# Performance work log

Measured on AMD Instinct MI355X. Metric: run time of the kernel, lower is better.

## Reference

```python
import jax, jax.numpy as jnp
import numpy as np

N_HEAD = 8
HEAD_DIM = 64  # d_model // n_head
NEG = -1000000000.0  # diagonal mask fill


def _rope(x):
    # x: [B, H, T, D], interleaved RoPE as in torch module
    T, D = x.shape[-2], x.shape[-1]
    theta = 1.0 / (10000.0 ** (jnp.arange(0, D, 2, dtype=jnp.float32) / D))  # [D/2]
    angle = jnp.arange(T, dtype=jnp.float32)[:, None] * theta[None, :]        # [T, D/2]
    cos, sin = jnp.cos(angle), jnp.sin(angle)
    x1, x2 = x[..., ::2], x[..., 1::2]
    # stack on last axis then flatten -> interleave
    out = jnp.stack([x1 * cos - x2 * sin, x1 * sin + x2 * cos], axis=-1)
    return out.reshape(x.shape)


def setup_inputs() -> dict:
    key = jax.random.key(0)
    k1, k2, k3 = jax.random.split(key, 3)
    B, T, C = 4, 2048, 512
    x = jax.random.normal(k1, (B, T, C), dtype=jnp.float32)
    w_qkv = jax.random.normal(k2, (C, 3 * C), dtype=jnp.float32) * 0.02
    w_proj = jax.random.normal(k3, (C, C), dtype=jnp.float32) * 0.02
    return {"x": x, "w_qkv": w_qkv, "w_proj": w_proj}


def reference(x, w_qkv, w_proj):
    B, T, C = x.shape
    H, D = N_HEAD, HEAD_DIM
    qkv = jnp.einsum('btc,cd->btd', x, w_qkv)
    q, k, v = jnp.split(qkv, 3, axis=-1)
    q = q.reshape(B, T, H, D).transpose(0, 2, 1, 3)
    k = k.reshape(B, T, H, D).transpose(0, 2, 1, 3)
    v = v.reshape(B, T, H, D).transpose(0, 2, 1, 3)
    q = _rope(q)
    k = _rope(k)
    scale = 1.0 / jnp.sqrt(jnp.float32(D))
    scores = jnp.einsum('bhqd,bhkd->bhqk', q, k) * scale
    mask = jnp.where(jnp.eye(T, dtype=bool), jnp.float32(NEG), jnp.float32(0.0))
    scores = scores + mask
    attn = jax.nn.softmax(scores, axis=-1)
    y = jnp.einsum('bhqk,bhkd->bhqd', attn, v)
    y = y.transpose(0, 2, 1, 3).reshape(B, T, C)
    return jnp.einsum('btc,cd->btd', y, w_proj)
```

## Files before the change

kernel.cpp:

```cpp
#include <hip/hip_runtime.h>

typedef unsigned short u16;
typedef __bf16 bf16x8 __attribute__((ext_vector_type(8)));
typedef float f32x4 __attribute__((ext_vector_type(4)));

#define B_ 4
#define T_ 2048
#define C_ 512
#define H_ 8
#define D_ 64

__device__ __forceinline__ u16 f2bf(float f) {
  unsigned u = __float_as_uint(f);
  unsigned r = (u + 0x7FFFu + ((u >> 16) & 1u)) >> 16;
  return (u16)r;
}
__device__ __forceinline__ float bf2f(unsigned h) {
  return __uint_as_float(h << 16);
}
__device__ __forceinline__ void gload16(const u16* g, u16* l) {
  __builtin_amdgcn_global_load_lds(
      (const __attribute__((address_space(1))) unsigned int*)g,
      (__attribute__((address_space(3))) unsigned int*)l, 16, 0, 0);
}

__global__ void cast4_kernel(const float* __restrict__ in, u16* __restrict__ out) {
  int i = blockIdx.x * blockDim.x + threadIdx.x;
  float4 v = ((const float4*)in)[i];
  unsigned lo = (unsigned)f2bf(v.x) | ((unsigned)f2bf(v.y) << 16);
  unsigned hi = (unsigned)f2bf(v.z) | ((unsigned)f2bf(v.w) << 16);
  ((uint2*)out)[i] = make_uint2(lo, hi);
}

__global__ void castT_kernel(const float* __restrict__ in, u16* __restrict__ outT,
                             int R, int Cc) {
  int i = blockIdx.x * blockDim.x + threadIdx.x;
  if (i >= R * Cc) return;
  int r = i / Cc, c = i - r * Cc;
  outT[c * R + r] = f2bf(in[i]);
}

__global__ void rope_table_kernel(float* __restrict__ cosT, float* __restrict__ sinT) {
  int i = blockIdx.x * blockDim.x + threadIdx.x;
  int t = i >> 5, p = i & 31;
  float theta = powf(10000.f, -(float)p / 32.f);
  float a = (float)t * theta;
  cosT[i] = cosf(a);
  sinT[i] = sinf(a);
}

__global__ void rope_kernel(u16* __restrict__ Qp, u16* __restrict__ Kp,
                            const float* __restrict__ cosT, const float* __restrict__ sinT) {
  int i = blockIdx.x * blockDim.x + threadIdx.x;
  int p = i & 31;
  int t = (i >> 5) & 2047;
  int bh = (i >> 16) & 31;
  u16* base = (i >> 21) ? Kp : Qp;
  unsigned off = ((unsigned)(bh * 2048 + t)) * 64u + (unsigned)(p * 2);
  unsigned v = *(const unsigned*)&base[off];
  int ti = (t << 5) + p;
  float c = cosT[ti], s = sinT[ti];
  float x1 = bf2f(v & 0xFFFFu), x2 = bf2f(v >> 16);
  float o1 = x1 * c - x2 * s;
  float o2 = x1 * s + x2 * c;
  *(unsigned*)&base[off] = (unsigned)f2bf(o1) | ((unsigned)f2bf(o2) << 16);
}

template <int EPI>
__global__ __launch_bounds__(256, 2)
void gemm_bt_kernel(const u16* __restrict__ A, const u16* __restrict__ BT,
                    int M, int N, int K, float* __restrict__ Cout,
                    u16* __restrict__ Qp, u16* __restrict__ Kp, u16* __restrict__ VTp) {
  __shared__ u16 As[128 * 64];
  __shared__ u16 Bs[128 * 64];
  const int tid = threadIdx.x;
  const int w = tid >> 6, l = tid & 63;
  const int m0 = blockIdx.x * 128, n0 = blockIdx.y * 128;
  const int wr = w >> 1, wc = w & 1;
  f32x4 acc[4][4] = {};

  const int srow = w * 32 + (l >> 3);
  const int scol = (l & 7) * 8;

  for (int k0 = 0; k0 < K; k0 += 64) {
#pragma unroll
    for (int c = 0; c < 4; ++c) {
      gload16(A + (m0 + srow + c * 8) * K + k0 + scol, &As[(w * 32 + c * 8) * 64]);
      gload16(BT + (n0 + srow + c * 8) * K + k0 + scol, &Bs[(w * 32 + c * 8) * 64]);
    }
    __syncthreads();
#pragma unroll
    for (int kk = 0; kk < 2; ++kk) {
      bf16x8 af[4], bfr[4];
#pragma unroll
      for (int i = 0; i < 4; ++i)
        af[i] = *(const bf16x8*)&As[(wr * 64 + i * 16 + (l & 15)) * 64 + kk * 32 + (l >> 4) * 8];
#pragma unroll
      for (int j = 0; j < 4; ++j)
        bfr[j] = *(const bf16x8*)&Bs[(wc * 64 + j * 16 + (l & 15)) * 64 + kk * 32 + (l >> 4) * 8];
#pragma unroll
      for (int i = 0; i < 4; ++i)
#pragma unroll
        for (int j = 0; j < 4; ++j)
          acc[i][j] = __builtin_amdgcn_mfma_f32_16x16x32_bf16(af[i], bfr[j], acc[i][j], 0, 0, 0);
    }
    __syncthreads();
  }

  const int mrow = wr * 64 + (l >> 4) * 4;
  const int ncol = wc * 64 + (l & 15);
  if (EPI == 1) {
#pragma unroll
    for (int i = 0; i < 4; ++i)
#pragma unroll
      for (int j = 0; j < 4; ++j)
#pragma unroll
        for (int r = 0; r < 4; ++r)
          Cout[(m0 + mrow + i * 16 + r) * N + (n0 + ncol + j * 16)] = acc[i][j][r];
  } else {
#pragma unroll
    for (int i = 0; i < 4; ++i) {
#pragma unroll
      for (int j = 0; j < 4; ++j) {
        int n = n0 + ncol + j * 16;
        int which = n >> 9;
        int hn = n & 511;
        int h = hn >> 6, d = hn & 63;
#pragma unroll
        for (int r = 0; r < 4; ++r) {
          int m = m0 + mrow + i * 16 + r;
          int b = m >> 11, t = m & 2047;
          int bh = b * 8 + h;
          u16 v = f2bf(acc[i][j][r]);
          if (which == 0)
            Qp[(bh * 2048 + t) * 64 + d] = v;
          else if (which == 1)
            Kp[(bh * 2048 + t) * 64 + d] = v;
          else
            VTp[(bh * 64 + d) * 2048 + t] = v;
        }
      }
    }
  }
}

__global__ __launch_bounds__(256, 2)
void attn_kernel(const u16* __restrict__ Qp, const u16* __restrict__ Kp,
                 const u16* __restrict__ VTp, u16* __restrict__ Yp) {
  __shared__ u16 Ks[64 * 64];
  __shared__ u16 Vs[64 * 64];
  __shared__ u16 Ps[4 * 16 * 64];
  const int tid = threadIdx.x;
  const int w = tid >> 6, l = tid & 63;
  const int qt = blockIdx.x, bh = blockIdx.y;
  const int b = bh >> 3, h = bh & 7;
  const int q0 = qt * 64;
  const u16* Qb = Qp + (bh * 2048 + q0) * 64;
  const u16* Kb = Kp + bh * 2048 * 64;
  const u16* Vb = VTp + bh * 64 * 2048;

  bf16x8 qf[2];
  {
    int row = w * 16 + (l & 15);
#pragma unroll
    for (int kk = 0; kk < 2; ++kk)
      qf[kk] = *(const bf16x8*)&Qb[row * 64 + kk * 32 + (l >> 4) * 8];
  }
  f32x4 o[4] = {};
  float dsum[4] = {0.f, 0.f, 0.f, 0.f};

  const int srow = w * 16 + (l >> 3);
  const int scol = ((l & 7) ^ (l >> 3)) * 8;
  const int rsw  = (l & 7) << 3;

  for (int kt = 0; kt < 32; ++kt) {
#pragma unroll
    for (int c = 0; c < 2; ++c) {
      gload16(Kb + (kt * 64 + srow + c * 8) * 64 + scol, &Ks[(w * 16 + c * 8) * 64]);
      gload16(Vb + (srow + c * 8) * 2048 + kt * 64 + scol, &Vs[(w * 16 + c * 8) * 64]);
    }
    __syncthreads();

#pragma unroll
    for (int nt = 0; nt < 4; ++nt) {
      f32x4 s = {0.f, 0.f, 0.f, 0.f};
#pragma unroll
      for (int kk = 0; kk < 2; ++kk) {
        bf16x8 kf = *(const bf16x8*)&Ks[(nt * 16 + (l & 15)) * 64 +
                                        ((kk * 32 + (l >> 4) * 8) ^ rsw)];
        s = __builtin_amdgcn_mfma_f32_16x16x32_bf16(qf[kk], kf, s, 0, 0, 0);
      }
      int key = kt * 64 + nt * 16 + (l & 15);
#pragma unroll
      for (int r = 0; r < 4; ++r) {
        int q = q0 + w * 16 + (l >> 4) * 4 + r;
        float p = (q == key) ? 0.f : __expf(s[r] * 0.125f);
        dsum[r] += p;
        int prow = w * 16 + (l >> 4) * 4 + r;
        Ps[prow * 64 + ((nt * 16 + (l & 15)) ^ ((prow & 7) << 3))] = f2bf(p);
      }
    }
    __syncthreads();

#pragma unroll
    for (int nt = 0; nt < 4; ++nt) {
#pragma unroll
      for (int kk = 0; kk < 2; ++kk) {
        bf16x8 pf = *(const bf16x8*)&Ps[(w * 16 + (l & 15)) * 64 +
                                        ((kk * 32 + (l >> 4) * 8) ^ rsw)];
        bf16x8 vf = *(const bf16x8*)&Vs[(nt * 16 + (l & 15)) * 64 +
                                        ((kk * 32 + (l >> 4) * 8) ^ rsw)];
        o[nt] = __builtin_amdgcn_mfma_f32_16x16x32_bf16(pf, vf, o[nt], 0, 0, 0);
      }
    }
    __syncthreads();
  }

#pragma unroll
  for (int m = 1; m < 16; m <<= 1)
#pragma unroll
    for (int r = 0; r < 4; ++r)
      dsum[r] += __shfl_xor(dsum[r], m, 64);

  float inv[4];
#pragma unroll
  for (int r = 0; r < 4; ++r) inv[r] = 1.f / dsum[r];

#pragma unroll
  for (int nt = 0; nt < 4; ++nt)
#pragma unroll
    for (int r = 0; r < 4; ++r) {
      int t = q0 + w * 16 + (l >> 4) * 4 + r;
      int cc = h * 64 + nt * 16 + (l & 15);
      Yp[(b * 2048 + t) * 512 + cc] = f2bf(o[nt][r] * inv[r]);
    }
}

extern "C" void kernel_launch(void* const* d_in, const int* in_sizes, int n_in,
                              void* d_out, int out_size, void* d_ws, size_t ws_size,
                              hipStream_t stream) {
  const float* x = (const float*)d_in[0];
  const float* wqkv = (const float*)d_in[1];
  const float* wproj = (const float*)d_in[2];
  float* out = (float*)d_out;
  char* ws = (char*)d_ws;

  u16* xb     = (u16*)(ws);
  u16* Yp     = (u16*)(ws);
  u16* wqkvT  = (u16*)(ws + 8388608);
  u16* wprojT = (u16*)(ws + 9961472);
  u16* Qp     = (u16*)(ws + 10485760);
  u16* Kp     = (u16*)(ws + 18874368);
  u16* VTp    = (u16*)(ws + 27262976);
  float* cosT = (float*)(ws + 35651584);
  float* sinT = (float*)(ws + 35913728);

  cast4_kernel<<<4096, 256, 0, stream>>>(x, xb);
  castT_kernel<<<3072, 256, 0, stream>>>(wqkv, wqkvT, 512, 1536);
  castT_kernel<<<1024, 256, 0, stream>>>(wproj, wprojT, 512, 512);
  rope_table_kernel<<<256, 256, 0, stream>>>(cosT, sinT);

  gemm_bt_kernel<0><<<dim3(64, 12), 256, 0, stream>>>(xb, wqkvT, 8192, 1536, 512,
                                                      nullptr, Qp, Kp, VTp);
  rope_kernel<<<16384, 256, 0, stream>>>(Qp, Kp, cosT, sinT);
  attn_kernel<<<dim3(32, 32), 256, 0, stream>>>(Qp, Kp, VTp, Yp);
  gemm_bt_kernel<1><<<dim3(64, 4), 256, 0, stream>>>(Yp, wprojT, 8192, 512, 512,
                                                     out, nullptr, nullptr, nullptr);
}
```

Measured before the change: 199.3 us.

## Double-buffer K/V tiles in attention and drop the mid-loop barrier

The attention loop now prefetches the next K/V tile into a second LDS buffer while the current tile is being computed, instead of loading and waiting at the top of each iteration. The barrier between writing P and reading it back is removed, since each wave only reads its own P rows. The diagonal-mask test now runs only on the diagonal tile. The weight-transpose cast kernel is also changed to write its output coalesced. The cost is double the LDS for K/V, which could reduce occupancy, and the design depends on the end-of-iteration barrier waiting for the async LDS loads.

```diff
diff --git a/kernel.cpp b/kernel.cpp
--- a/kernel.cpp
+++ b/kernel.cpp
@@ -36,8 +36,8 @@
                              int R, int Cc) {
   int i = blockIdx.x * blockDim.x + threadIdx.x;
   if (i >= R * Cc) return;
-  int r = i / Cc, c = i - r * Cc;
-  outT[c * R + r] = f2bf(in[i]);
+  int c = i / R, r = i - c * R;
+  outT[i] = f2bf(in[r * Cc + c]);
 }
 
 __global__ void rope_table_kernel(float* __restrict__ cosT, float* __restrict__ sinT) {
@@ -147,8 +147,8 @@
 __global__ __launch_bounds__(256, 2)
 void attn_kernel(const u16* __restrict__ Qp, const u16* __restrict__ Kp,
                  const u16* __restrict__ VTp, u16* __restrict__ Yp) {
-  __shared__ u16 Ks[64 * 64];
-  __shared__ u16 Vs[64 * 64];
+  __shared__ u16 Ks[2][64 * 64];
+  __shared__ u16 Vs[2][64 * 64];
   __shared__ u16 Ps[4 * 16 * 64];
   const int tid = threadIdx.x;
   const int w = tid >> 6, l = tid & 63;
@@ -173,34 +173,44 @@
   const int scol = ((l & 7) ^ (l >> 3)) * 8;
   const int rsw  = (l & 7) << 3;
 
+#define STAGE(kt, bb)                                                            \
+  do {                                                                           \
+    _Pragma("unroll")                                                            \
+    for (int c = 0; c < 2; ++c) {                                                \
+      gload16(Kb + ((kt) * 64 + srow + c * 8) * 64 + scol,                       \
+              &Ks[bb][(w * 16 + c * 8) * 64]);                                   \
+      gload16(Vb + (srow + c * 8) * 2048 + (kt) * 64 + scol,                     \
+              &Vs[bb][(w * 16 + c * 8) * 64]);                                   \
+    }                                                                            \
+  } while (0)
+
+  STAGE(0, 0);
+  __syncthreads();
+
+  int cur = 0;
   for (int kt = 0; kt < 32; ++kt) {
-#pragma unroll
-    for (int c = 0; c < 2; ++c) {
-      gload16(Kb + (kt * 64 + srow + c * 8) * 64 + scol, &Ks[(w * 16 + c * 8) * 64]);
-      gload16(Vb + (srow + c * 8) * 2048 + kt * 64 + scol, &Vs[(w * 16 + c * 8) * 64]);
-    }
-    __syncthreads();
+    if (kt < 31) STAGE(kt + 1, cur ^ 1);
+    const bool diagtile = (kt == qt);
 
 #pragma unroll
     for (int nt = 0; nt < 4; ++nt) {
       f32x4 s = {0.f, 0.f, 0.f, 0.f};
 #pragma unroll
       for (int kk = 0; kk < 2; ++kk) {
-        bf16x8 kf = *(const bf16x8*)&Ks[(nt * 16 + (l & 15)) * 64 +
-                                        ((kk * 32 + (l >> 4) * 8) ^ rsw)];
+        bf16x8 kf = *(const bf16x8*)&Ks[cur][(nt * 16 + (l & 15)) * 64 +
+                                           ((kk * 32 + (l >> 4) * 8) ^ rsw)];
         s = __builtin_amdgcn_mfma_f32_16x16x32_bf16(qf[kk], kf, s, 0, 0, 0);
       }
-      int key = kt * 64 + nt * 16 + (l & 15);
+      int keyi = nt * 16 + (l & 15);
 #pragma unroll
       for (int r = 0; r < 4; ++r) {
-        int q = q0 + w * 16 + (l >> 4) * 4 + r;
-        float p = (q == key) ? 0.f : __expf(s[r] * 0.125f);
-        dsum[r] += p;
-        int prow = w * 16 + (l >> 4) * 4 + r;
-        Ps[prow * 64 + ((nt * 16 + (l & 15)) ^ ((prow & 7) << 3))] = f2bf(p);
-      }
-    }
-    __syncthreads();
+        int qrow = w * 16 + (l >> 4) * 4 + r;
+        float e = __expf(s[r] * 0.125f);
+        if (diagtile && (qrow == keyi)) e = 0.f;
+        dsum[r] += e;
+        Ps[qrow * 64 + (keyi ^ ((qrow & 7) << 3))] = f2bf(e);
+      }
+    }
 
 #pragma unroll
     for (int nt = 0; nt < 4; ++nt) {
@@ -208,13 +218,15 @@
       for (int kk = 0; kk < 2; ++kk) {
         bf16x8 pf = *(const bf16x8*)&Ps[(w * 16 + (l & 15)) * 64 +
                                         ((kk * 32 + (l >> 4) * 8) ^ rsw)];
-        bf16x8 vf = *(const bf16x8*)&Vs[(nt * 16 + (l & 15)) * 64 +
-                                        ((kk * 32 + (l >> 4) * 8) ^ rsw)];
+        bf16x8 vf = *(const bf16x8*)&Vs[cur][(nt * 16 + (l & 15)) * 64 +
+                                            ((kk * 32 + (l >> 4) * 8) ^ rsw)];
         o[nt] = __builtin_amdgcn_mfma_f32_16x16x32_bf16(pf, vf, o[nt], 0, 0, 0);
       }
     }
     __syncthreads();
-  }
+    cur ^= 1;
+  }
+#undef STAGE
 
 #pragma unroll
   for (int m = 1; m < 16; m <<= 1)
```

After: 194.8 us. -2.2%, faster.
